# Performance work log

Measured on AMD Instinct MI355X. Metric: run time of the kernel, lower is better.

## Reference

```python
import jax, jax.numpy as jnp
import numpy as np

jax.config.update("jax_enable_x64", True)

STRIDE = 1
PADDING = 1


def _im2col(x, k, s):
    # x: (n, c, H, W) already padded. Returns (n, c*k*k, oh*ow) with
    # channel-major, then (kh, kw) ordering -- matching torch unfold/img2col.
    n, c, H, W = x.shape
    oh = (H - k) // s + 1
    ow = (W - k) // s + 1
    # k*k = 9 slices: small fixed loop over kernel offsets, fully vectorized
    # over batch/channel/spatial dims.
    patches = jnp.stack(
        [x[:, :, i:i + s * (oh - 1) + 1:s, j:j + s * (ow - 1) + 1:s]
         for i in range(k) for j in range(k)],
        axis=2,
    )  # (n, c, k*k, oh, ow)
    return patches.reshape(n, c * k * k, oh * ow)


def setup_inputs() -> dict:
    key = jax.random.key(0)
    k1, k2, k3 = jax.random.split(key, 3)
    x = jax.random.randint(k1, (32, 64, 56, 56), 0, 65536, dtype=jnp.int64)
    weight = jax.random.randint(k2, (64, 64, 3, 3), 0, 65536, dtype=jnp.int64)
    bias = jax.random.randint(k3, (64,), 0, 65536, dtype=jnp.int64)
    return {"x": x, "weight": weight, "bias": bias}


def reference(x, weight, bias):
    kN, kC, k, _ = weight.shape
    n, c, H, W = x.shape
    oh = (H - k + 2 * PADDING) // STRIDE + 1
    ow = (W - k + 2 * PADDING) // STRIDE + 1
    # pad spatial dims with zeros (ring zero)
    xp = jnp.pad(x, ((0, 0), (0, 0), (PADDING, PADDING), (PADDING, PADDING)))
    cols = _im2col(xp, k, STRIDE)              # (n, c*k*k, L)
    cols_t = cols.transpose(0, 2, 1)           # (n, L, c*k*k)
    w2 = weight.reshape(kN, kC * k * k).T      # (c*k*k, kN)
    # int64 matmul: overflow wraps (two's complement), matching ring Z_{2^64}
    out = jnp.einsum('nlk,ko->nlo', cols_t, w2) + bias  # (n, L, kN)
    return out.transpose(0, 2, 1).reshape(n, kN, oh, ow)
```

## Files before the change

kernel.cpp:

```cpp
#include <hip/hip_runtime.h>


typedef int v4i __attribute__((ext_vector_type(4)));

#define LCOL 144
#define LROW (58 * LCOL)

__device__ __align__(16) unsigned char g_wb[2 * 9 * 64 * 64];
__device__ unsigned g_off[64];

static __device__ __forceinline__ unsigned bsum(unsigned v, unsigned acc) {
#if __has_builtin(__builtin_amdgcn_sad_u8)
    return __builtin_amdgcn_sad_u8(v, 0u, acc);
#else
    return acc + (v & 0xFFu) + ((v >> 8) & 0xFFu) + ((v >> 16) & 0xFFu) + (v >> 24);
#endif
}

__global__ __launch_bounds__(256) void packw(const int* __restrict__ w,
                                             const int* __restrict__ bias) {
    int blk = blockIdx.x;
    if (blk < 144) {
        int i = blk * 256 + threadIdx.x;
        if (i >= 64 * 64 * 9) return;
        int k = i / 576;
        int r = i - k * 576;
        int c = r / 9;
        int t = r - c * 9;
        unsigned v = (unsigned)w[i];
        g_wb[((0 * 9 + t) * 64 + k) * 64 + c] = (unsigned char)((v & 255u) ^ 0x80u);
        g_wb[((1 * 9 + t) * 64 + k) * 64 + c] = (unsigned char)(((v >> 8) & 255u) ^ 0x80u);
    } else if (threadIdx.x < 64) {
        int k = threadIdx.x;
        int s0 = 0, s1 = 0;
        for (int j = 0; j < 576; ++j) {
            unsigned W = (unsigned)w[k * 576 + j];
            s0 += (int)(W & 255u);
            s1 += (int)((W >> 8) & 255u);
        }
        s0 -= 73728;
        s1 -= 73728;
        unsigned ws = (unsigned)(s0 + 256 * s1);
        g_off[k] = (unsigned)bias[k] + 32896u * ws + 1082146816u * 576u;
    }
}

__global__ __launch_bounds__(256, 2) void secconv(const int* __restrict__ x,
                                                  int* __restrict__ out)
{
    __shared__ unsigned char sx[4 * LROW];
    __shared__ int ss[232];

    const int tid  = threadIdx.x;
    const int blk  = blockIdx.x;
    const int q    = blk >> 3;
    const int rp   = q % 28;
    const int n    = (blk & 7) + 8 * (q / 28);
    const int wid  = tid >> 6;
    const int lane = tid & 63;
    const int lm   = lane & 15;
    const int lq   = lane >> 4;
    const int kp   = wid & 1;
    const int ph   = wid >> 1;
    const int kbase = kp * 32;

    if (tid < 232) {
        const int pr = tid / 58, pc = tid - pr * 58;
        const int ih = 2 * rp - 1 + pr, iw = pc - 1;
        unsigned char* ob = sx + pr * LROW + pc * LCOL;
        int S;
        if ((unsigned)ih < 56u && (unsigned)iw < 56u) {
            const int* xp = x + (long)n * 64 * 3136 + ih * 56 + iw;
            unsigned slo = 0, shi = 0;
#pragma unroll
            for (int g = 0; g < 4; ++g) {
                unsigned lo[4], hi[4];
#pragma unroll
                for (int u = 0; u < 4; ++u) {
                    const int c = g * 16 + u * 4;
                    unsigned v0 = (unsigned)xp[(c + 0) * 3136];
                    unsigned v1 = (unsigned)xp[(c + 1) * 3136];
                    unsigned v2 = (unsigned)xp[(c + 2) * 3136];
                    unsigned v3 = (unsigned)xp[(c + 3) * 3136];
                    unsigned t01 = __builtin_amdgcn_perm(v1, v0, 0x05040100u);
                    unsigned t23 = __builtin_amdgcn_perm(v3, v2, 0x05040100u);
                    unsigned lw  = __builtin_amdgcn_perm(t23, t01, 0x06040200u);
                    unsigned hw  = __builtin_amdgcn_perm(t23, t01, 0x07050301u);
                    slo = bsum(lw, slo);
                    shi = bsum(hw, shi);
                    lo[u] = lw ^ 0x80808080u;
                    hi[u] = hw ^ 0x80808080u;
                }
                *(uint4*)(ob + g * 16)      = make_uint4(lo[0], lo[1], lo[2], lo[3]);
                *(uint4*)(ob + 64 + g * 16) = make_uint4(hi[0], hi[1], hi[2], hi[3]);
            }
            S = (int)(slo + (shi << 8)) - 2105344;
        } else {
            uint4 v = make_uint4(0x80808080u, 0x80808080u, 0x80808080u, 0x80808080u);
#pragma unroll
            for (int g = 0; g < 4; ++g) {
                *(uint4*)(ob + g * 16)      = v;
                *(uint4*)(ob + 64 + g * 16) = v;
            }
            S = -2105344;
        }
        ss[tid] = S;
    }

    v4i wf[2][2][9];
#pragma unroll
    for (int kt = 0; kt < 2; ++kt)
#pragma unroll
        for (int l = 0; l < 2; ++l)
#pragma unroll
            for (int t = 0; t < 9; ++t)
                wf[kt][l][t] = *(const v4i*)(g_wb +
                    ((l * 9 + t) * 64 + (kbase + kt * 16 + lm)) * 64 + lq * 16);
    unsigned offv[2][4];
#pragma unroll
    for (int kt = 0; kt < 2; ++kt)
#pragma unroll
        for (int r = 0; r < 4; ++r)
            offv[kt][r] = g_off[kbase + kt * 16 + lq * 4 + r];

    __syncthreads();

    const int r8 = lm >> 3, c8 = lm & 7;
    const unsigned char* lbase = sx + r8 * LROW + c8 * LCOL + lq * 16;

    const int t0 = ph ? 4 : 0, t1 = ph ? 7 : 4;
    for (int t = t0; t < t1; ++t) {
        const unsigned char* tb = lbase + t * 8 * LCOL;
        v4i a00[2] = {{0,0,0,0},{0,0,0,0}}, a01[2] = {{0,0,0,0},{0,0,0,0}};
        v4i a10[2] = {{0,0,0,0},{0,0,0,0}}, a11[2] = {{0,0,0,0},{0,0,0,0}};
#pragma unroll
        for (int tap = 0; tap < 9; ++tap) {
            const int dr = tap / 3, dc = tap - (tap / 3) * 3;
            const unsigned char* pp = tb + dr * LROW + dc * LCOL;
            v4i bl = *(const v4i*)(pp);
            v4i bh = *(const v4i*)(pp + 64);
#pragma unroll
            for (int kt = 0; kt < 2; ++kt) {
                a00[kt] = __builtin_amdgcn_mfma_i32_16x16x64_i8(wf[kt][0][tap], bl, a00[kt], 0, 0, 0);
                a01[kt] = __builtin_amdgcn_mfma_i32_16x16x64_i8(wf[kt][0][tap], bh, a01[kt], 0, 0, 0);
                a10[kt] = __builtin_amdgcn_mfma_i32_16x16x64_i8(wf[kt][1][tap], bl, a10[kt], 0, 0, 0);
                a11[kt] = __builtin_amdgcn_mfma_i32_16x16x64_i8(wf[kt][1][tap], bh, a11[kt], 0, 0, 0);
            }
        }

        const int pc = t * 8 + c8;
        int Q = 0;
#pragma unroll
        for (int dr = 0; dr < 3; ++dr)
#pragma unroll
            for (int dc = 0; dc < 3; ++dc)
                Q += ss[(r8 + dr) * 58 + pc + dc];
        const unsigned qq = 32896u * (unsigned)Q;

        const long pix = (long)(2 * rp + r8) * 56 + pc;
#pragma unroll
        for (int kt = 0; kt < 2; ++kt) {
            const long ob = ((long)n * 64 + kbase + kt * 16 + lq * 4) * 3136 + pix;
#pragma unroll
            for (int r = 0; r < 4; ++r) {
                unsigned val = (unsigned)a00[kt][r]
                             + (((unsigned)a01[kt][r] + (unsigned)a10[kt][r]) << 8)
                             + ((unsigned)a11[kt][r] << 16)
                             + qq + offv[kt][r];
                out[ob + (long)r * 3136] = (int)val;
            }
        }
    }
}

extern "C" void kernel_launch(void* const* d_in, const int* in_sizes, int n_in,
                              void* d_out, int out_size, void* d_ws, size_t ws_size,
                              hipStream_t stream)
{
    const int* x    = (const int*)d_in[0];
    const int* w    = (const int*)d_in[1];
    const int* bias = (const int*)d_in[2];
    int* out        = (int*)d_out;

    packw  <<<dim3(145), dim3(256), 0, stream>>>(w, bias);
    secconv<<<dim3(896), dim3(256), 0, stream>>>(x, out);
}
```

Measured before the change: 108.7 us.

## Process four output rows per block to cut halo reloads; parallelize weight sums

Each conv block now covers four output rows instead of two. It stages six padded input rows in LDS instead of four, so the redundant halo loads and byte-split conversion work per output row drop, and the grid is halved to 448 blocks. The wave split changes from column halves to row pairs, so each wave loops over all seven column tiles. The weight-offset reduction in packw is also spread over four threads per output channel with shuffle reductions. The cost is 50% more LDS per block, which may lower occupancy, and fewer blocks to spread across the CUs.

```diff
diff --git a/kernel.cpp b/kernel.cpp
--- a/kernel.cpp
+++ b/kernel.cpp
@@ -30,32 +30,37 @@
         unsigned v = (unsigned)w[i];
         g_wb[((0 * 9 + t) * 64 + k) * 64 + c] = (unsigned char)((v & 255u) ^ 0x80u);
         g_wb[((1 * 9 + t) * 64 + k) * 64 + c] = (unsigned char)(((v >> 8) & 255u) ^ 0x80u);
-    } else if (threadIdx.x < 64) {
-        int k = threadIdx.x;
+    } else {
+        int k    = threadIdx.x >> 2;
+        int part = threadIdx.x & 3;
         int s0 = 0, s1 = 0;
-        for (int j = 0; j < 576; ++j) {
+        for (int j = part * 144; j < part * 144 + 144; ++j) {
             unsigned W = (unsigned)w[k * 576 + j];
             s0 += (int)(W & 255u);
             s1 += (int)((W >> 8) & 255u);
         }
-        s0 -= 73728;
-        s1 -= 73728;
-        unsigned ws = (unsigned)(s0 + 256 * s1);
-        g_off[k] = (unsigned)bias[k] + 32896u * ws + 1082146816u * 576u;
+        s0 += __shfl_xor(s0, 1); s0 += __shfl_xor(s0, 2);
+        s1 += __shfl_xor(s1, 1); s1 += __shfl_xor(s1, 2);
+        if (part == 0) {
+            s0 -= 73728;
+            s1 -= 73728;
+            unsigned ws = (unsigned)(s0 + 256 * s1);
+            g_off[k] = (unsigned)bias[k] + 32896u * ws + 1082146816u * 576u;
+        }
     }
 }
 
 __global__ __launch_bounds__(256, 2) void secconv(const int* __restrict__ x,
                                                   int* __restrict__ out)
 {
-    __shared__ unsigned char sx[4 * LROW];
-    __shared__ int ss[232];
+    __shared__ unsigned char sx[6 * LROW];
+    __shared__ int ss[6 * 58];
 
     const int tid  = threadIdx.x;
     const int blk  = blockIdx.x;
     const int q    = blk >> 3;
-    const int rp   = q % 28;
-    const int n    = (blk & 7) + 8 * (q / 28);
+    const int rg   = q % 14;
+    const int n    = (blk & 7) + 8 * (q / 14);
     const int wid  = tid >> 6;
     const int lane = tid & 63;
     const int lm   = lane & 15;
@@ -64,9 +69,9 @@
     const int ph   = wid >> 1;
     const int kbase = kp * 32;
 
-    if (tid < 232) {
-        const int pr = tid / 58, pc = tid - pr * 58;
-        const int ih = 2 * rp - 1 + pr, iw = pc - 1;
+    for (int it = tid; it < 348; it += 256) {
+        const int pr = it / 58, pc = it - pr * 58;
+        const int ih = 4 * rg - 1 + pr, iw = pc - 1;
         unsigned char* ob = sx + pr * LROW + pc * LCOL;
         int S;
         if ((unsigned)ih < 56u && (unsigned)iw < 56u) {
@@ -104,7 +109,7 @@
             }
             S = -2105344;
         }
-        ss[tid] = S;
+        ss[it] = S;
     }
 
     v4i wf[2][2][9];
@@ -126,10 +131,10 @@
     __syncthreads();
 
     const int r8 = lm >> 3, c8 = lm & 7;
-    const unsigned char* lbase = sx + r8 * LROW + c8 * LCOL + lq * 16;
+    const int lrow = 2 * ph + r8;
+    const unsigned char* lbase = sx + lrow * LROW + c8 * LCOL + lq * 16;
 
-    const int t0 = ph ? 4 : 0, t1 = ph ? 7 : 4;
-    for (int t = t0; t < t1; ++t) {
+    for (int t = 0; t < 7; ++t) {
         const unsigned char* tb = lbase + t * 8 * LCOL;
         v4i a00[2] = {{0,0,0,0},{0,0,0,0}}, a01[2] = {{0,0,0,0},{0,0,0,0}};
         v4i a10[2] = {{0,0,0,0},{0,0,0,0}}, a11[2] = {{0,0,0,0},{0,0,0,0}};
@@ -154,10 +159,10 @@
         for (int dr = 0; dr < 3; ++dr)
 #pragma unroll
             for (int dc = 0; dc < 3; ++dc)
-                Q += ss[(r8 + dr) * 58 + pc + dc];
+                Q += ss[(lrow + dr) * 58 + pc + dc];
         const unsigned qq = 32896u * (unsigned)Q;
 
-        const long pix = (long)(2 * rp + r8) * 56 + pc;
+        const long pix = (long)(4 * rg + lrow) * 56 + pc;
 #pragma unroll
         for (int kt = 0; kt < 2; ++kt) {
             const long ob = ((long)n * 64 + kbase + kt * 16 + lq * 4) * 3136 + pix;
@@ -183,5 +188,5 @@
     int* out        = (int*)d_out;
 
     packw  <<<dim3(145), dim3(256), 0, stream>>>(w, bias);
-    secconv<<<dim3(896), dim3(256), 0, stream>>>(x, out);
+    secconv<<<dim3(448), dim3(256), 0, stream>>>(x, out);
 }
```

Result: faster. 98.57 us (-9.3%).
